# Kernel optimization log

Measured on AMD Instinct MI355X. Metric: run time of the kernel, lower is better.

## Reference

```python
import jax, jax.numpy as jnp
import numpy as np

D_IN = 3
HID = 256
N_BRANCH = 8
SKIP_IN = (4,)
CSG_TREE = [0, 1, [2, 3], [4, 5, [6, 7]]]
FLAG_CONVEX = True
BETA = 100.0
N_POINTS = 100000

# layer dims: [3, 256*7, 8]; layer whose OUTPUT feeds a skip layer emits 256-3=253
_DIMS = [D_IN] + [HID] * 7 + [N_BRANCH]


def _layer_out_dim(layer):
    if (layer + 1) in SKIP_IN:
        return _DIMS[layer + 1] - D_IN
    return _DIMS[layer + 1]


def setup_inputs() -> dict:
    key = jax.random.key(0)
    keys = jax.random.split(key, 20)
    inp = {"x": jax.random.normal(keys[0], (N_POINTS, D_IN), dtype=jnp.float32)}
    n_layers = len(_DIMS) - 1  # 8 linear layers
    for layer in range(n_layers):
        in_d = _DIMS[layer]
        out_d = _layer_out_dim(layer)
        kw = jax.random.fold_in(keys[1], layer)
        if layer == n_layers - 1:  # geometric init of last layer
            W = (np.sqrt(np.pi) / np.sqrt(in_d)
                 + 1e-5 * jax.random.normal(kw, (in_d, out_d), dtype=jnp.float32))
            b = -1.0 * jnp.ones((out_d,), dtype=jnp.float32)
        else:
            W = (np.sqrt(2.0) / np.sqrt(out_d)) * jax.random.normal(
                kw, (in_d, out_d), dtype=jnp.float32)
            b = jnp.zeros((out_d,), dtype=jnp.float32)
        inp[f"W{layer}"] = W
        inp[f"b{layer}"] = b
    return inp


def _softplus_beta(x):
    return jax.nn.softplus(BETA * x) / BETA


def _csg_combine(vals, ops, cvx_flag):
    # hard CSG tree: one-hot matmul == column gather; recursion is static (trace time)
    idxs = [v for v in ops if not isinstance(v, list)]
    cols = [vals[:, jnp.array(idxs)]]
    for v in ops:
        if isinstance(v, list):
            cols.append(_csg_combine(vals, v, not cvx_flag))
    m = jnp.concatenate(cols, axis=1)
    red = jnp.max if cvx_flag else jnp.min
    return red(m, axis=1, keepdims=True)


def _forward(x, Ws, bs):
    inp = x
    h = x
    n_layers = len(Ws)
    inv_sqrt2 = np.float32(1.0 / np.sqrt(2.0))
    for layer in range(n_layers):
        if layer in SKIP_IN:
            h = jnp.concatenate([h, inp], axis=-1) * inv_sqrt2
        h = h @ Ws[layer] + bs[layer]
        if layer < n_layers - 1:
            h = _softplus_beta(h)
    branch_vals = h  # [N, n_branch]
    hcsg = _csg_combine(branch_vals, CSG_TREE, FLAG_CONVEX)  # [N, 1]
    return jnp.concatenate([hcsg, branch_vals], axis=1)  # flag_output == 0


def reference(x, W0, b0, W1, b1, W2, b2, W3, b3, W4, b4, W5, b5, W6, b6, W7, b7):
    Ws = [W0, W1, W2, W3, W4, W5, W6, W7]
    bs = [b0, b1, b2, b3, b4, b5, b6, b7]
    return _forward(x, Ws, bs)
```

## Files before the change

### kernel.cpp

```cpp
#include <hip/hip_runtime.h>
#include <hip/hip_bf16.h>


using bf16x8 = __attribute__((ext_vector_type(8))) __bf16;
using f32x4  = __attribute__((ext_vector_type(4))) float;

#define LDA 264

#define OFFW0 0
#define OFFW1 8192
#define OFFW2 73728
#define OFFW3 139264
#define OFFW4 204800
#define OFFW5 270336
#define OFFW6 335872
#define OFFW7 401408
#define WSB_BYTE_OFF 811008
#define OFFB7 1792

#define SCALE_T2 144.26950408889634f
#define INV_SQRT2 0.70710678118654752f
#define LN2_100 0.0069314718055994531f

__device__ __forceinline__ float fast_exp2(float x) {
#if __has_builtin(__builtin_amdgcn_exp2f)
    return __builtin_amdgcn_exp2f(x);
#else
    return exp2f(x);
#endif
}
__device__ __forceinline__ float fast_log2(float x) {
#if __has_builtin(__builtin_amdgcn_logf)
    return __builtin_amdgcn_logf(x);
#else
    return log2f(x);
#endif
}

__device__ __forceinline__ float softplus_t2(float t2) {
    float e = fast_exp2(-fabsf(t2));
    float l = fast_log2(1.0f + e);
    return fmaxf(t2, 0.0f) + l;
}

__device__ __forceinline__ unsigned short bf16_rne(float f) {
    unsigned int u = __float_as_uint(f);
    unsigned int r = u + 0x7FFFu + ((u >> 16) & 1u);
    return (unsigned short)(r >> 16);
}

template <int KK, int MODE>
__device__ __forceinline__ void layer_mm(
    const unsigned short* __restrict__ wfrag,
    const float* __restrict__ bias,
    unsigned short* act, const float* xst,
    int wave, int lane)
{
    const int quad = lane >> 4;
    const int l15  = lane & 15;

    f32x4 acc[2][3];
#pragma unroll
    for (int i = 0; i < 2; ++i) {
        const int chb = (wave * 2 + i) * 16 + quad * 4;
        const float4 b4 = *(const float4*)(bias + chb);
#pragma unroll
        for (int nt = 0; nt < 3; ++nt)
            acc[i][nt] = f32x4{b4.x, b4.y, b4.z, b4.w};
    }

    const unsigned short* wbase = wfrag + (wave * 2 * KK * 64 + lane) * 8;

#pragma unroll
    for (int kk = 0; kk < KK; ++kk) {
        bf16x8 bfr[3];
#pragma unroll
        for (int nt = 0; nt < 3; ++nt)
            bfr[nt] = *(const bf16x8*)(act + (nt * 16 + l15) * LDA + kk * 32 + quad * 8);
#pragma unroll
        for (int i = 0; i < 2; ++i) {
            bf16x8 afr = *(const bf16x8*)(wbase + (i * KK + kk) * 512);
#pragma unroll
            for (int nt = 0; nt < 3; ++nt)
                acc[i][nt] = __builtin_amdgcn_mfma_f32_16x16x32_bf16(afr, bfr[nt], acc[i][nt], 0, 0, 0);
        }
    }

    __syncthreads();

#pragma unroll
    for (int i = 0; i < 2; ++i) {
        const int chb = (wave * 2 + i) * 16 + quad * 4;
#pragma unroll
        for (int nt = 0; nt < 3; ++nt) {
            const int pt = nt * 16 + l15;
            float vv[4];
#pragma unroll
            for (int r = 0; r < 4; ++r) {
                float s = softplus_t2(acc[i][nt][r]);
                if (MODE == 1) {
                    const int ch = chb + r;
                    if (ch >= 253)
                        s = xst[pt * 4 + (ch - 253)];
                }
                vv[r] = s;
            }
            __hip_bfloat162 p01 = __float22bfloat162_rn(float2{vv[0], vv[1]});
            __hip_bfloat162 p23 = __float22bfloat162_rn(float2{vv[2], vv[3]});
            uint2 pk;
            pk.x = *(unsigned int*)&p01;
            pk.y = *(unsigned int*)&p23;
            *(uint2*)(act + pt * LDA + chb) = pk;
        }
    }

    __syncthreads();
}

__global__ __launch_bounds__(512, 8)
void nhrep_main(const float* __restrict__ x, float* __restrict__ out,
                const unsigned short* __restrict__ wsW,
                const float* __restrict__ wsB, int npts)
{
    __shared__ unsigned short act[48 * LDA];
    __shared__ float xst[48 * 4];
    const int tid  = threadIdx.x;
    const int wave = tid >> 6, lane = tid & 63;
    const int quad = lane >> 4, l15 = lane & 15;
    const int base_pt = blockIdx.x * 48;

    for (int i = tid; i < 48 * 32; i += 512) {
        const int pt = i >> 5, ch = i & 31;
        const int ptg = base_pt + pt;
        float v = 0.0f;
        if (ch < 3 && ptg < npts) v = x[ptg * 3 + ch];
        act[pt * LDA + ch] = bf16_rne(v);
        if (ch < 4) xst[pt * 4 + ch] = (ch < 3) ? v : 0.0f;
    }
    __syncthreads();

    layer_mm<1, 0>(wsW + OFFW0, wsB + 0 * 256, act, xst, wave, lane);
    layer_mm<8, 0>(wsW + OFFW1, wsB + 1 * 256, act, xst, wave, lane);
    layer_mm<8, 0>(wsW + OFFW2, wsB + 2 * 256, act, xst, wave, lane);
    layer_mm<8, 1>(wsW + OFFW3, wsB + 3 * 256, act, xst, wave, lane);
    layer_mm<8, 0>(wsW + OFFW4, wsB + 4 * 256, act, xst, wave, lane);
    layer_mm<8, 0>(wsW + OFFW5, wsB + 5 * 256, act, xst, wave, lane);
    layer_mm<8, 0>(wsW + OFFW6, wsB + 6 * 256, act, xst, wave, lane);

    if (wave < 3) {
        const float4 b4 = *(const float4*)(wsB + OFFB7 + quad * 4);
        f32x4 acc = f32x4{b4.x, b4.y, b4.z, b4.w};
        const unsigned short* w7 = wsW + OFFW7;
#pragma unroll
        for (int kk = 0; kk < 8; ++kk) {
            bf16x8 bfr = *(const bf16x8*)(act + (wave * 16 + l15) * LDA + kk * 32 + quad * 8);
            bf16x8 afr = *(const bf16x8*)(w7 + (kk * 64 + lane) * 8);
            acc = __builtin_amdgcn_mfma_f32_16x16x32_bf16(afr, bfr, acc, 0, 0, 0);
        }
        float u0 = __shfl(acc[0], l15 + 16);
        float u1 = __shfl(acc[1], l15 + 16);
        float u2 = __shfl(acc[2], l15 + 16);
        float u3 = __shfl(acc[3], l15 + 16);
        if (quad == 0) {
            const int ptg = base_pt + wave * 16 + l15;
            if (ptg < npts) {
                const float v0 = acc[0], v1 = acc[1], v2 = acc[2], v3 = acc[3];
                const float v4 = u0, v5 = u1, v6 = u2, v7 = u3;
                const float m23   = fminf(v2, v3);
                const float m67   = fmaxf(v6, v7);
                const float m4567 = fminf(fminf(v4, v5), m67);
                const float h     = fmaxf(fmaxf(v0, v1), fmaxf(m23, m4567));
                float* o = out + (long)ptg * 9;
                o[0] = h;
                o[1] = v0; o[2] = v1; o[3] = v2; o[4] = v3;
                o[5] = v4; o[6] = v5; o[7] = v6; o[8] = v7;
            }
        }
    }
}

struct PackArgs {
    const float* W[8];
    const float* b[8];
};

#define TOTAL_FRAGS 50688
#define TOTAL_BIAS  1808

__global__ void prepack_all(PackArgs args, unsigned short* __restrict__ dstW,
                            float* __restrict__ dstB)
{
    const int t = blockIdx.x * blockDim.x + threadIdx.x;
    const int FB[9]  = {0, 1024, 9216, 17408, 25600, 33792, 41984, 50176, 50688};
    const int KKs[8] = {1, 8, 8, 8, 8, 8, 8, 8};
    const int ind[8] = {3, 256, 256, 256, 256, 256, 256, 256};
    const int outd[8]= {256, 256, 256, 253, 256, 256, 256, 8};

    if (t < TOTAL_FRAGS) {
        int l = 0;
        while (t >= FB[l + 1]) ++l;
        const int f    = t - FB[l];
        const int lane = f & 63;
        const int kk   = (f >> 6) % KKs[l];
        const int mt   = f / (64 * KKs[l]);
        const int o    = mt * 16 + (lane & 15);
        const int kb   = kk * 32 + (lane >> 4) * 8;
        const float* W = args.W[l];
        const int in_d = ind[l], out_d = outd[l];

        unsigned short v[8];
#pragma unroll
        for (int j = 0; j < 8; ++j) {
            const int k = kb + j;
            float w = 0.0f;
            if (k < in_d && o < out_d) {
                float sc = 1.0f;
                if (l == 0) sc = SCALE_T2;
                else if (l == 4) sc = (k < 253) ? INV_SQRT2 : (SCALE_T2 * INV_SQRT2);
                else if (l == 7) sc = LN2_100;
                w = W[k * out_d + o] * sc;
            }
            unsigned int u = __float_as_uint(w);
            v[j] = (unsigned short)((u + 0x7FFFu + ((u >> 16) & 1u)) >> 16);
        }
        uint4 p;
        p.x = (unsigned int)v[0] | ((unsigned int)v[1] << 16);
        p.y = (unsigned int)v[2] | ((unsigned int)v[3] << 16);
        p.z = (unsigned int)v[4] | ((unsigned int)v[5] << 16);
        p.w = (unsigned int)v[6] | ((unsigned int)v[7] << 16);
        *(uint4*)(dstW + (long)t * 8) = p;
    } else if (t < TOTAL_FRAGS + TOTAL_BIAS) {
        const int u = t - TOTAL_FRAGS;
        const int l = (u < 1792) ? (u >> 8) : 7;
        const int idx = (l < 7) ? (u & 255) : (u - 1792);
        const float sc = (l < 7) ? SCALE_T2 : 1.0f;
        dstB[u] = (idx < outd[l]) ? args.b[l][idx] * sc : 0.0f;
    }
}

extern "C" void kernel_launch(void* const* d_in, const int* in_sizes, int n_in,
                              void* d_out, int out_size, void* d_ws, size_t ws_size,
                              hipStream_t stream)
{
    const float* x = (const float*)d_in[0];
    unsigned short* wsW = (unsigned short*)d_ws;
    float* wsB = (float*)((char*)d_ws + WSB_BYTE_OFF);

    PackArgs pa;
    for (int l = 0; l < 8; ++l) {
        pa.W[l] = (const float*)d_in[1 + 2 * l];
        pa.b[l] = (const float*)d_in[2 + 2 * l];
    }
    const int ptot = TOTAL_FRAGS + TOTAL_BIAS;
    prepack_all<<<(ptot + 255) / 256, 256, 0, stream>>>(pa, wsW, wsB);

    const int npts = in_sizes[0] / 3;
    const int nblk = (npts + 47) / 48;
    nhrep_main<<<nblk, 512, 0, stream>>>(x, (float*)d_out, wsW, wsB, npts);
}
```

Before: 215.0 us.

## Ping-pong two point tiles per block to overlap softplus epilogue with MFMA

```diff
diff --git a/kernel.cpp b/kernel.cpp
--- a/kernel.cpp
+++ b/kernel.cpp
@@ -9,11 +9,6 @@
 
 #define OFFW0 0
 #define OFFW1 8192
-#define OFFW2 73728
-#define OFFW3 139264
-#define OFFW4 204800
-#define OFFW5 270336
-#define OFFW6 335872
 #define OFFW7 401408
 #define WSB_BYTE_OFF 811008
 #define OFFB7 1792
@@ -49,111 +44,150 @@
     return (unsigned short)(r >> 16);
 }
 
-template <int KK, int MODE>
-__device__ __forceinline__ void layer_mm(
-    const unsigned short* __restrict__ wfrag,
-    const float* __restrict__ bias,
-    unsigned short* act, const float* xst,
+__device__ __forceinline__ void epi_chunk(
+    f32x4 (&acc)[2][3], int i, int nt,
+    unsigned short* dst, const float* xst, bool splice,
     int wave, int lane)
 {
     const int quad = lane >> 4;
     const int l15  = lane & 15;
-
-    f32x4 acc[2][3];
+    const int chb  = (wave * 2 + i) * 16 + quad * 4;
+    const int pt   = nt * 16 + l15;
+    float vv[4];
+#pragma unroll
+    for (int r = 0; r < 4; ++r) {
+        float s = softplus_t2(acc[i][nt][r]);
+        if (splice) {
+            const int ch = chb + r;
+            if (ch >= 253)
+                s = xst[pt * 4 + (ch - 253)];
+        }
+        vv[r] = s;
+    }
+    __hip_bfloat162 p01 = __float22bfloat162_rn(float2{vv[0], vv[1]});
+    __hip_bfloat162 p23 = __float22bfloat162_rn(float2{vv[2], vv[3]});
+    uint2 pk;
+    pk.x = *(unsigned int*)&p01;
+    pk.y = *(unsigned int*)&p23;
+    *(uint2*)(dst + pt * LDA + chb) = pk;
+}
+
+template <int KK, bool EPI>
+__device__ __forceinline__ void region(
+    const unsigned short* __restrict__ wfragA, const float* __restrict__ biasA,
+    const unsigned short* __restrict__ actA, f32x4 (&accA)[2][3],
+    unsigned short* actB, const float* xstB, f32x4 (&accB)[2][3], bool spliceB,
+    int wave, int lane)
+{
+    const int quad = lane >> 4;
+    const int l15  = lane & 15;
+
 #pragma unroll
     for (int i = 0; i < 2; ++i) {
         const int chb = (wave * 2 + i) * 16 + quad * 4;
-        const float4 b4 = *(const float4*)(bias + chb);
+        const float4 b4 = *(const float4*)(biasA + chb);
 #pragma unroll
         for (int nt = 0; nt < 3; ++nt)
-            acc[i][nt] = f32x4{b4.x, b4.y, b4.z, b4.w};
-    }
-
-    const unsigned short* wbase = wfrag + (wave * 2 * KK * 64 + lane) * 8;
+            accA[i][nt] = f32x4{b4.x, b4.y, b4.z, b4.w};
+    }
+
+    const unsigned short* wbase = wfragA + (wave * 2 * KK * 64 + lane) * 8;
 
 #pragma unroll
     for (int kk = 0; kk < KK; ++kk) {
         bf16x8 bfr[3];
 #pragma unroll
         for (int nt = 0; nt < 3; ++nt)
-            bfr[nt] = *(const bf16x8*)(act + (nt * 16 + l15) * LDA + kk * 32 + quad * 8);
+            bfr[nt] = *(const bf16x8*)(actA + (nt * 16 + l15) * LDA + kk * 32 + quad * 8);
 #pragma unroll
         for (int i = 0; i < 2; ++i) {
             bf16x8 afr = *(const bf16x8*)(wbase + (i * KK + kk) * 512);
 #pragma unroll
             for (int nt = 0; nt < 3; ++nt)
-                acc[i][nt] = __builtin_amdgcn_mfma_f32_16x16x32_bf16(afr, bfr[nt], acc[i][nt], 0, 0, 0);
-        }
-    }
-
-    __syncthreads();
-
-#pragma unroll
-    for (int i = 0; i < 2; ++i) {
-        const int chb = (wave * 2 + i) * 16 + quad * 4;
-#pragma unroll
-        for (int nt = 0; nt < 3; ++nt) {
-            const int pt = nt * 16 + l15;
-            float vv[4];
-#pragma unroll
-            for (int r = 0; r < 4; ++r) {
-                float s = softplus_t2(acc[i][nt][r]);
-                if (MODE == 1) {
-                    const int ch = chb + r;
-                    if (ch >= 253)
-                        s = xst[pt * 4 + (ch - 253)];
-                }
-                vv[r] = s;
-            }
-            __hip_bfloat162 p01 = __float22bfloat162_rn(float2{vv[0], vv[1]});
-            __hip_bfloat162 p23 = __float22bfloat162_rn(float2{vv[2], vv[3]});
-            uint2 pk;
-            pk.x = *(unsigned int*)&p01;
-            pk.y = *(unsigned int*)&p23;
-            *(uint2*)(act + pt * LDA + chb) = pk;
-        }
-    }
-
-    __syncthreads();
-}
-
-__global__ __launch_bounds__(512, 8)
+                accA[i][nt] = __builtin_amdgcn_mfma_f32_16x16x32_bf16(afr, bfr[nt], accA[i][nt], 0, 0, 0);
+        }
+        if (EPI && kk < 6)
+            epi_chunk(accB, kk & 1, kk >> 1, actB, xstB, spliceB, wave, lane);
+    }
+    if (EPI && KK == 1) {
+#pragma unroll
+        for (int c = 1; c < 6; ++c)
+            epi_chunk(accB, c & 1, c >> 1, actB, xstB, spliceB, wave, lane);
+    }
+}
+
+__device__ __forceinline__ void epi_all(
+    f32x4 (&acc)[2][3], unsigned short* dst, const float* xst, bool splice,
+    int wave, int lane)
+{
+#pragma unroll
+    for (int c = 0; c < 6; ++c)
+        epi_chunk(acc, c & 1, c >> 1, dst, xst, splice, wave, lane);
+}
+
+__global__ __launch_bounds__(512, 4)
 void nhrep_main(const float* __restrict__ x, float* __restrict__ out,
                 const unsigned short* __restrict__ wsW,
                 const float* __restrict__ wsB, int npts)
 {
-    __shared__ unsigned short act[48 * LDA];
-    __shared__ float xst[48 * 4];
+    __shared__ unsigned short actT0[48 * LDA];
+    __shared__ unsigned short actT1[48 * LDA];
+    __shared__ float xst[96 * 4];
     const int tid  = threadIdx.x;
     const int wave = tid >> 6, lane = tid & 63;
     const int quad = lane >> 4, l15 = lane & 15;
-    const int base_pt = blockIdx.x * 48;
-
-    for (int i = tid; i < 48 * 32; i += 512) {
+    const int base_pt = blockIdx.x * 96;
+
+    for (int i = tid; i < 96 * 32; i += 512) {
         const int pt = i >> 5, ch = i & 31;
         const int ptg = base_pt + pt;
         float v = 0.0f;
         if (ch < 3 && ptg < npts) v = x[ptg * 3 + ch];
-        act[pt * LDA + ch] = bf16_rne(v);
+        unsigned short* dst = (pt < 48) ? (actT0 + pt * LDA + ch)
+                                        : (actT1 + (pt - 48) * LDA + ch);
+        *dst = bf16_rne(v);
         if (ch < 4) xst[pt * 4 + ch] = (ch < 3) ? v : 0.0f;
     }
     __syncthreads();
 
-    layer_mm<1, 0>(wsW + OFFW0, wsB + 0 * 256, act, xst, wave, lane);
-    layer_mm<8, 0>(wsW + OFFW1, wsB + 1 * 256, act, xst, wave, lane);
-    layer_mm<8, 0>(wsW + OFFW2, wsB + 2 * 256, act, xst, wave, lane);
-    layer_mm<8, 1>(wsW + OFFW3, wsB + 3 * 256, act, xst, wave, lane);
-    layer_mm<8, 0>(wsW + OFFW4, wsB + 4 * 256, act, xst, wave, lane);
-    layer_mm<8, 0>(wsW + OFFW5, wsB + 5 * 256, act, xst, wave, lane);
-    layer_mm<8, 0>(wsW + OFFW6, wsB + 6 * 256, act, xst, wave, lane);
-
-    if (wave < 3) {
+    f32x4 acc0[2][3], acc1[2][3];
+    const float* xst0 = xst;
+    const float* xst1 = xst + 48 * 4;
+
+    region<1, false>(wsW + OFFW0, wsB, actT0, acc0,
+                     actT1, xst1, acc1, false, wave, lane);
+    __syncthreads();
+    region<1, true>(wsW + OFFW0, wsB, actT1, acc1,
+                    actT0, xst0, acc0, false, wave, lane);
+    __syncthreads();
+
+#pragma unroll 1
+    for (int l = 1; l <= 6; ++l) {
+        const unsigned short* wl = wsW + OFFW1 + (l - 1) * 65536;
+        const float* bl = wsB + l * 256;
+        region<8, true>(wl, bl, actT0, acc0,
+                        actT1, xst1, acc1, (l - 1) == 3, wave, lane);
+        __syncthreads();
+        region<8, true>(wl, bl, actT1, acc1,
+                        actT0, xst0, acc0, l == 3, wave, lane);
+        __syncthreads();
+    }
+
+    epi_all(acc1, actT1, xst1, false, wave, lane);
+    __syncthreads();
+
+    if (wave < 6) {
+        const bool t0 = wave < 3;
+        const unsigned short* act = t0 ? actT0 : actT1;
+        const int wl = t0 ? wave : wave - 3;
+        const int pbase = base_pt + (t0 ? 0 : 48) + wl * 16;
+
         const float4 b4 = *(const float4*)(wsB + OFFB7 + quad * 4);
         f32x4 acc = f32x4{b4.x, b4.y, b4.z, b4.w};
         const unsigned short* w7 = wsW + OFFW7;
 #pragma unroll
         for (int kk = 0; kk < 8; ++kk) {
-            bf16x8 bfr = *(const bf16x8*)(act + (wave * 16 + l15) * LDA + kk * 32 + quad * 8);
+            bf16x8 bfr = *(const bf16x8*)(act + (wl * 16 + l15) * LDA + kk * 32 + quad * 8);
             bf16x8 afr = *(const bf16x8*)(w7 + (kk * 64 + lane) * 8);
             acc = __builtin_amdgcn_mfma_f32_16x16x32_bf16(afr, bfr, acc, 0, 0, 0);
         }
@@ -162,7 +196,7 @@
         float u2 = __shfl(acc[2], l15 + 16);
         float u3 = __shfl(acc[3], l15 + 16);
         if (quad == 0) {
-            const int ptg = base_pt + wave * 16 + l15;
+            const int ptg = pbase + l15;
             if (ptg < npts) {
                 const float v0 = acc[0], v1 = acc[1], v2 = acc[2], v3 = acc[3];
                 const float v4 = u0, v5 = u1, v6 = u2, v7 = u3;
@@ -255,6 +289,6 @@
     prepack_all<<<(ptot + 255) / 256, 256, 0, stream>>>(pa, wsW, wsB);
 
     const int npts = in_sizes[0] / 3;
-    const int nblk = (npts + 47) / 48;
+    const int nblk = (npts + 95) / 96;
     nhrep_main<<<nblk, 512, 0, stream>>>(x, (float*)d_out, wsW, wsB, npts);
 }
```

New measurement: 253.4 us. 17.9% more time.
